# Performance work log

Hardware: AMD Instinct MI355X
Metric: run time of the kernel (lower is better)

The kernel has to match this reference:

```python
import jax, jax.numpy as jnp
import numpy as np

KEY_SIZE = 512


def setup_inputs() -> dict:
    key = jax.random.key(0)
    ks = jax.random.split(key, 4)
    B, T, C = 8, 2048, 512
    s = 0.02
    return {
        "x": jax.random.normal(ks[0], (B, T, C), dtype=jnp.float32),
        "Wq": jax.random.normal(ks[1], (KEY_SIZE, C), dtype=jnp.float32) * s,
        "bq": jnp.zeros((KEY_SIZE,), dtype=jnp.float32),
        "Wk": jax.random.normal(ks[2], (KEY_SIZE, C), dtype=jnp.float32) * s,
        "bk": jnp.zeros((KEY_SIZE,), dtype=jnp.float32),
        "Wv": jax.random.normal(ks[3], (KEY_SIZE, C), dtype=jnp.float32) * s,
        "bv": jnp.zeros((KEY_SIZE,), dtype=jnp.float32),
    }


def reference(x, Wq, bq, Wk, bk, Wv, bv):
    # x: [B, T, C]; Linear(y) = y @ W.T + b (torch convention)
    q = jnp.einsum("btc,kc->btk", x, Wq) + bq  # [B, T, K]
    k = jnp.einsum("btc,kc->btk", x, Wk) + bk  # [B, T, K]
    v = jnp.einsum("btc,vc->btv", x, Wv) + bv  # [B, T, V]

    scores = jnp.einsum("bqk,bsk->bqs", q, k)  # [B, Tq, Tk]
    T = x.shape[1]
    # mask[j, i] = 1 if i > j  -> strict upper triangle masked with -inf
    mask = jnp.triu(jnp.ones((T, T), dtype=bool), k=1)
    scores = jnp.where(mask[None, :, :], -jnp.inf, scores)
    # NOTE: original divides by sqrt(key_size) AFTER masking, and takes
    # softmax over dim=1 (the QUERY axis) — faithfully reproduced.
    probs = jax.nn.softmax(scores / jnp.sqrt(jnp.asarray(KEY_SIZE, scores.dtype)), axis=1)
    attn = jnp.einsum("bqs,bsv->bqv", probs, v)  # [B, T, V]
    return jnp.concatenate([x, attn], axis=2)  # [B, T, C + V]
```

## Files before the change

kernel.cpp:

```cpp
#include <hip/hip_runtime.h>

#define BATCH 8
#define TSEQ  2048
#define CDIM  512
#define MTOK  (BATCH*TSEQ)
#define NTRI  136

typedef __attribute__((ext_vector_type(8))) short bf16x8;
typedef __attribute__((ext_vector_type(4))) float f32x4;

__device__ __forceinline__ unsigned short f2bf(float f) {
    union { float f; unsigned int u; } v; v.f = f;
    unsigned int r = v.u + 0x7FFF + ((v.u >> 16) & 1);
    return (unsigned short)(r >> 16);
}
__device__ __forceinline__ float bfl(unsigned short u) {
    union { unsigned int i; float f; } v; v.i = ((unsigned int)u) << 16; return v.f;
}

__device__ __forceinline__ f32x4 fzero() { f32x4 z = {0.f, 0.f, 0.f, 0.f}; return z; }

__device__ __forceinline__ void gl2lds16(const void* g, void* l) {
    __builtin_amdgcn_global_load_lds(
        (const __attribute__((address_space(1))) unsigned int*)g,
        (__attribute__((address_space(3))) unsigned int*)l, 16, 0, 0);
}

__device__ __forceinline__ void stage_tile(const unsigned short* src, size_t ld,
                                           unsigned short* buf, int t) {
    const unsigned short* s0 = src + (size_t)(t >> 2) * ld + (t & 3) * 8;
    gl2lds16(s0, &buf[t * 8]);
    gl2lds16(s0 + (size_t)64 * ld, &buf[2048 + t * 8]);
}

__global__ __launch_bounds__(256) void k_convert_x(const float* __restrict__ x,
                                                   unsigned short* __restrict__ xb,
                                                   float* __restrict__ out) {
    int i = blockIdx.x * blockDim.x + threadIdx.x;
    float4 v = ((const float4*)x)[i];
    ushort4 o;
    o.x = f2bf(v.x); o.y = f2bf(v.y); o.z = f2bf(v.z); o.w = f2bf(v.w);
    ((ushort4*)xb)[i] = o;
    int e = i * 4;
    int row = e >> 9;
    int c   = e & 511;
    *(float4*)(out + (size_t)row * 1024 + c) = v;
}

__global__ __launch_bounds__(256) void k_convert_w3(const float* __restrict__ Wq,
                                                    const float* __restrict__ Wk,
                                                    const float* __restrict__ Wv,
                                                    unsigned short* __restrict__ wb) {
    int i = blockIdx.x * 256 + threadIdx.x;
    int m = i >> 16;
    const float* w = (m == 0) ? Wq : ((m == 1) ? Wk : Wv);
    float4 v = ((const float4*)w)[i & 65535];
    ushort4 o;
    o.x = f2bf(v.x); o.y = f2bf(v.y); o.z = f2bf(v.z); o.w = f2bf(v.w);
    ((ushort4*)wb)[i] = o;
}

__global__ __launch_bounds__(512, 2) void k_qkv(const unsigned short* __restrict__ xb,
                                                const unsigned short* __restrict__ Wcat,
                                                const float* __restrict__ bq,
                                                const float* __restrict__ bk,
                                                const float* __restrict__ bv,
                                                unsigned short* __restrict__ QKb,
                                                unsigned short* __restrict__ Vt) {
    __shared__ __align__(16) unsigned short lds[65536];
    int orig = blockIdx.x;
    int flat = (orig & 7) * 48 + (orig >> 3);
    int mt = flat / 6, nt = flat - mt * 6;
    int m0 = mt * 256, n0 = nt * 256;
    int t = threadIdx.x, w = t >> 6, lane = t & 63;
    int quad = lane >> 4, lane16 = lane & 15;
    int wr = w >> 2, wc = w & 3;
    int l3 = lane >> 3;
    int sl = (lane & 7) ^ l3;
    int rswz = (lane16 & 7) << 3;

    const unsigned short* Abase = xb + (size_t)m0 * 512;
    const unsigned short* Bbase = Wcat + (size_t)n0 * 512;

    f32x4 acc[8][4];
#pragma unroll
    for (int i = 0; i < 8; i++)
#pragma unroll
        for (int j = 0; j < 4; j++) acc[i][j] = fzero();

    auto stage = [&](const unsigned short* src, unsigned short* buf) {
#pragma unroll
        for (int i = 0; i < 4; ++i) {
            int q = i * 8 + w;
            gl2lds16(src + (size_t)(q * 8 + l3) * 512 + sl * 8,
                     &buf[q * 512 + lane * 8]);
        }
    };

    stage(Abase, &lds[0]);
    stage(Bbase, &lds[16384]);
    __syncthreads();

#pragma unroll
    for (int kt = 0; kt < 8; ++kt) {
        int c = kt & 1;
        if (kt + 1 < 8) {
            stage(Abase + (kt + 1) * 64, &lds[(c ^ 1) * 32768]);
            stage(Bbase + (kt + 1) * 64, &lds[(c ^ 1) * 32768 + 16384]);
        }
        const unsigned short* As = &lds[c * 32768];
        const unsigned short* Bs = As + 16384;

        bf16x8 bfr[4][2];
#pragma unroll
        for (int ni = 0; ni < 4; ++ni) {
            int row = wc * 64 + ni * 16 + lane16;
#pragma unroll
            for (int ks = 0; ks < 2; ++ks)
                bfr[ni][ks] = *(const bf16x8*)&Bs[row * 64 + ((ks * 32 + quad * 8) ^ rswz)];
        }
#pragma unroll
        for (int mh = 0; mh < 2; ++mh) {
            bf16x8 afr[4][2];
#pragma unroll
            for (int mi2 = 0; mi2 < 4; ++mi2) {
                int row = wr * 128 + mh * 64 + mi2 * 16 + lane16;
#pragma unroll
                for (int ks = 0; ks < 2; ++ks)
                    afr[mi2][ks] = *(const bf16x8*)&As[row * 64 + ((ks * 32 + quad * 8) ^ rswz)];
            }
            __builtin_amdgcn_s_setprio(1);
#pragma unroll
            for (int mi2 = 0; mi2 < 4; ++mi2)
#pragma unroll
                for (int ni = 0; ni < 4; ++ni)
#pragma unroll
                    for (int ks = 0; ks < 2; ++ks)
                        acc[mh * 4 + mi2][ni] = __builtin_amdgcn_mfma_f32_16x16x32_bf16(
                            afr[mi2][ks], bfr[ni][ks], acc[mh * 4 + mi2][ni], 0, 0, 0);
            __builtin_amdgcn_s_setprio(0);
        }
        __syncthreads();
    }

    int which = n0 >> 9;
    if (which < 2) {
        const float* bias = which ? bk : bq;
        unsigned short* T = &lds[w * 4608];
        int colBase = which * 512 + (n0 & 511) + wc * 64;
#pragma unroll
        for (int p = 0; p < 2; ++p) {
#pragma unroll
            for (int ni = 0; ni < 4; ++ni) {
                float bb = bias[(n0 & 511) + wc * 64 + ni * 16 + lane16];
#pragma unroll
                for (int mi2 = 0; mi2 < 4; ++mi2)
#pragma unroll
                    for (int r = 0; r < 4; ++r)
                        T[(mi2 * 16 + quad * 4 + r) * 72 + ni * 16 + lane16] =
                            f2bf(acc[p * 4 + mi2][ni][r] + bb);
            }
#pragma unroll
            for (int i = 0; i < 8; ++i) {
                int rl = i * 8 + l3;
                int cl = (lane & 7) * 8;
                int m = m0 + wr * 128 + p * 64 + rl;
                *(uint4*)(QKb + (size_t)m * 1024 + colBase + cl) = *(const uint4*)&T[rl * 72 + cl];
            }
        }
    } else {
        unsigned short* T = &lds[w * 4352];
        int b = m0 >> 11, tbase = (m0 & 2047) + wr * 128;
        int nv = (n0 & 511) + wc * 64;
#pragma unroll
        for (int p = 0; p < 2; ++p) {
#pragma unroll
            for (int j = 0; j < 2; ++j) {
                int ni = p * 2 + j;
                float bb = bv[nv + ni * 16 + lane16];
                int vl = j * 16 + lane16;
#pragma unroll
                for (int mi = 0; mi < 8; ++mi)
#pragma unroll
                    for (int r = 0; r < 4; ++r)
                        T[vl * 136 + mi * 16 + quad * 4 + r] = f2bf(acc[mi][ni][r] + bb);
            }
#pragma unroll
            for (int i = 0; i < 8; ++i) {
                int vl = i * 4 + quad;
                int tl = lane16 * 8;
                int v = nv + p * 32 + vl;
                *(uint4*)(Vt + ((size_t)(b * 512 + v)) * 2048 + tbase + tl) =
                    *(const uint4*)&T[vl * 136 + tl];
            }
        }
    }
}

__global__ __launch_bounds__(256) void k_score(const unsigned short* __restrict__ QKb,
                                               unsigned short* __restrict__ Pbuf,
                                               float* __restrict__ colsum) {
    __shared__ __align__(16) unsigned short lds[16384];
    int orig = blockIdx.x;
    int bb  = orig & 7;
    int idx = orig >> 3;
    int qt = (int)((sqrtf(8.0f * idx + 1.0f) - 1.0f) * 0.5f);
    while ((qt + 1) * (qt + 2) / 2 <= idx) qt++;
    while (qt * (qt + 1) / 2 > idx) qt--;
    int st = idx - qt * (qt + 1) / 2;
    int q0 = qt * 128, s0 = st * 128;

    int t = threadIdx.x, w = t >> 6, lane = t & 63, quad = lane >> 4, lane16 = lane & 15;
    int rowHalf = (w >> 1) * 64, colHalf = (w & 1) * 64;
    const unsigned short* Qrows = QKb + ((size_t)(bb * 2048 + q0)) * 1024;
    const unsigned short* Krows = QKb + ((size_t)(bb * 2048 + s0)) * 1024 + 512;

    f32x4 acc[4][4];
#pragma unroll
    for (int i = 0; i < 4; i++)
#pragma unroll
        for (int j = 0; j < 4; j++) acc[i][j] = fzero();

    stage_tile(Qrows, 1024, lds, t);
    stage_tile(Krows, 1024, lds + 4096, t);
    __syncthreads();
    int cur = 0;
    for (int k0 = 0; k0 < CDIM; k0 += 32) {
        unsigned short* As = lds + cur * 8192;
        unsigned short* Bs = As + 4096;
        if (k0 + 32 < CDIM) {
            unsigned short* An = lds + (cur ^ 1) * 8192;
            stage_tile(Qrows + k0 + 32, 1024, An, t);
            stage_tile(Krows + k0 + 32, 1024, An + 4096, t);
        }
        bf16x8 a[4], b[4];
#pragma unroll
        for (int mi = 0; mi < 4; mi++)
            a[mi] = *(const bf16x8*)&As[(rowHalf + mi * 16 + lane16) * 32 + quad * 8];
#pragma unroll
        for (int ni = 0; ni < 4; ni++)
            b[ni] = *(const bf16x8*)&Bs[(colHalf + ni * 16 + lane16) * 32 + quad * 8];
#pragma unroll
        for (int mi = 0; mi < 4; mi++)
#pragma unroll
            for (int ni = 0; ni < 4; ni++)
                acc[mi][ni] = __builtin_amdgcn_mfma_f32_16x16x32_bf16(a[mi], b[ni], acc[mi][ni], 0, 0, 0);
        __syncthreads();
        cur ^= 1;
    }

    const float scale = 0.044194173824159216f;
    unsigned short* T = &lds[w * 4096];
    float csum[4] = {0.f, 0.f, 0.f, 0.f};
#pragma unroll
    for (int ni = 0; ni < 4; ni++) {
        int s = s0 + colHalf + ni * 16 + lane16;
#pragma unroll
        for (int mi = 0; mi < 4; mi++)
#pragma unroll
            for (int r = 0; r < 4; r++) {
                int q = q0 + rowHalf + mi * 16 + quad * 4 + r;
                float p = 0.0f;
                if (s <= q) { p = __expf(acc[mi][ni][r] * scale); csum[ni] += p; }
                T[(mi * 16 + quad * 4 + r) * 64 + ni * 16 + lane16] = f2bf(p);
            }
    }
#pragma unroll
    for (int ni = 0; ni < 4; ni++) {
        float v = csum[ni];
        v += __shfl_xor(v, 16);
        v += __shfl_xor(v, 32);
        if (quad == 0)
            unsafeAtomicAdd(&colsum[bb * 2048 + s0 + colHalf + ni * 16 + lane16], v);
    }
    __syncthreads();
    unsigned short* tile = Pbuf + ((size_t)(bb * NTRI + idx)) * 16384;
#pragma unroll
    for (int i = 0; i < 8; i++) {
        int rl = i * 8 + (lane >> 3);
        int cl = (lane & 7) * 8;
        *(uint4*)(tile + (rowHalf + rl) * 128 + colHalf + cl) = *(const uint4*)&T[rl * 64 + cl];
    }
}

__global__ __launch_bounds__(256) void k_invcs(float* __restrict__ cs) {
    int i = blockIdx.x * 256 + threadIdx.x;
    cs[i] = 1.0f / cs[i];
}

__global__ __launch_bounds__(256) void k_vscale(unsigned short* __restrict__ Vt,
                                                const float* __restrict__ inv) {
    int idx = blockIdx.x * 256 + threadIdx.x;
    int s8  = idx & 255;
    int row = idx >> 8;
    int b   = row >> 9;
    uint4 raw = ((const uint4*)Vt)[idx];
    const float* ip = inv + b * TSEQ + s8 * 8;
    unsigned int rr[4] = {raw.x, raw.y, raw.z, raw.w};
    unsigned int oo[4];
#pragma unroll
    for (int j = 0; j < 4; j++) {
        float f0 = bfl((unsigned short)(rr[j] & 0xffff)) * ip[j * 2];
        float f1 = bfl((unsigned short)(rr[j] >> 16))    * ip[j * 2 + 1];
        oo[j] = (unsigned int)f2bf(f0) | ((unsigned int)f2bf(f1) << 16);
    }
    uint4 o = {oo[0], oo[1], oo[2], oo[3]};
    ((uint4*)Vt)[idx] = o;
}

__global__ __launch_bounds__(256) void k_attn(const unsigned short* __restrict__ Pbuf,
                                              const unsigned short* __restrict__ Vt,
                                              float* __restrict__ out) {
    __shared__ __align__(16) unsigned short lds[16384];
    int i = blockIdx.x;
    int slot = i & 255, half = i >> 8;
    int qt = half ? (15 - (slot >> 5)) : (slot >> 5);
    int bv = slot & 31;
    int bb = bv >> 2;
    int v0 = (bv & 3) * 128;
    int t = threadIdx.x, w = t >> 6, lane = t & 63, quad = lane >> 4, lane16 = lane & 15;
    int rowHalf = (w >> 1) * 64, colHalf = (w & 1) * 64;

    const unsigned short* Pb = Pbuf + ((size_t)(bb * NTRI + qt * (qt + 1) / 2)) * 16384;
    const unsigned short* Vb = Vt + ((size_t)(bb * 512 + v0)) * 2048;

    f32x4 acc[4][4];
#pragma unroll
    for (int ii = 0; ii < 4; ii++)
#pragma unroll
        for (int j = 0; j < 4; j++) acc[ii][j] = fzero();

    int Kend = (qt + 1) * 128;
    stage_tile(Pb, 128, lds, t);
    stage_tile(Vb, 2048, lds + 4096, t);
    __syncthreads();
    int cur = 0;
    for (int k0 = 0; k0 < Kend; k0 += 32) {
        unsigned short* As = lds + cur * 8192;
        unsigned short* Bs = As + 4096;
        int k1 = k0 + 32;
        if (k1 < Kend) {
            unsigned short* An = lds + (cur ^ 1) * 8192;
            stage_tile(Pb + (size_t)(k1 >> 7) * 16384 + (k1 & 127), 128, An, t);
            stage_tile(Vb + k1, 2048, An + 4096, t);
        }
        bf16x8 a[4], b[4];
#pragma unroll
        for (int mi = 0; mi < 4; mi++)
            a[mi] = *(const bf16x8*)&As[(rowHalf + mi * 16 + lane16) * 32 + quad * 8];
#pragma unroll
        for (int ni = 0; ni < 4; ni++)
            b[ni] = *(const bf16x8*)&Bs[(colHalf + ni * 16 + lane16) * 32 + quad * 8];
#pragma unroll
        for (int mi = 0; mi < 4; mi++)
#pragma unroll
            for (int ni = 0; ni < 4; ni++)
                acc[mi][ni] = __builtin_amdgcn_mfma_f32_16x16x32_bf16(a[mi], b[ni], acc[mi][ni], 0, 0, 0);
        __syncthreads();
        cur ^= 1;
    }

#pragma unroll
    for (int mi = 0; mi < 4; mi++)
#pragma unroll
        for (int ni = 0; ni < 4; ni++)
#pragma unroll
            for (int r = 0; r < 4; r++) {
                int q = qt * 128 + rowHalf + mi * 16 + quad * 4 + r;
                int v = v0 + colHalf + ni * 16 + lane16;
                out[((size_t)(bb * 2048 + q)) * 1024 + 512 + v] = acc[mi][ni][r];
            }
}

extern "C" void kernel_launch(void* const* d_in, const int* in_sizes, int n_in,
                              void* d_out, int out_size, void* d_ws, size_t ws_size,
                              hipStream_t stream) {
    const float* x  = (const float*)d_in[0];
    const float* Wq = (const float*)d_in[1];
    const float* bq = (const float*)d_in[2];
    const float* Wk = (const float*)d_in[3];
    const float* bk = (const float*)d_in[4];
    const float* Wv = (const float*)d_in[5];
    const float* bv = (const float*)d_in[6];
    float* out = (float*)d_out;

    char* ws = (char*)d_ws;
    size_t off = 0;
    auto alloc = [&](size_t bytes) -> void* {
        void* p = ws + off;
        off += (bytes + 255) & ~(size_t)255;
        return p;
    };
    unsigned short* QKb = (unsigned short*)alloc((size_t)MTOK * 1024 * 2);
    unsigned short* Vt  = (unsigned short*)alloc((size_t)MTOK * CDIM * 2);
    float* colsum = (float*)alloc((size_t)BATCH * TSEQ * 4);
    size_t mark = off;
    unsigned short* Wcat = (unsigned short*)alloc((size_t)3 * CDIM * CDIM * 2);
    unsigned short* xb   = (unsigned short*)alloc((size_t)MTOK * CDIM * 2);
    unsigned short* Pbuf = (unsigned short*)(ws + mark);
    (void)ws_size;

    k_convert_x<<<(MTOK * CDIM / 4) / 256, 256, 0, stream>>>(x, xb, out);
    k_convert_w3<<<(3 * CDIM * CDIM / 4) / 256, 256, 0, stream>>>(Wq, Wk, Wv, Wcat);

    k_qkv<<<384, 512, 0, stream>>>(xb, Wcat, bq, bk, bv, QKb, Vt);

    hipMemsetAsync(colsum, 0, (size_t)BATCH * TSEQ * 4, stream);
    k_score<<<1088, 256, 0, stream>>>(QKb, Pbuf, colsum);

    k_invcs<<<(BATCH * TSEQ) / 256, 256, 0, stream>>>(colsum);
    k_vscale<<<(MTOK * CDIM / 8) / 256, 256, 0, stream>>>(Vt, colsum);

    k_attn<<<512, 256, 0, stream>>>(Pbuf, Vt, out);
}
```

Measured before the change: 217.3 us.

## Restructure QKV projection GEMM main loop into fine-grained half-tile pipelined schedule

Rewrites the QKV projection GEMM K-loop as an 8-wave ping-pong style schedule. Loads are staged in half-tiles interleaved between four quadrant MFMA blocks, with explicit vmcnt/lgkmcnt waits and sched barriers. The goal is to overlap global-to-LDS loads and LDS fragment reads with MFMA work instead of staging whole tiles and syncing once per K step. It also adds a syncthreads in the V-transpose epilogue. The cost is many more barriers per iteration and a hand-tuned wait count scheme that could stall or race if miscounted.

```diff
diff --git a/kernel.cpp b/kernel.cpp
--- a/kernel.cpp
+++ b/kernel.cpp
@@ -32,6 +32,14 @@
     gl2lds16(s0, &buf[t * 8]);
     gl2lds16(s0 + (size_t)64 * ld, &buf[2048 + t * 8]);
 }
+
+#define LGKM0() do { asm volatile("s_waitcnt lgkmcnt(0)" ::: "memory"); \
+                     __builtin_amdgcn_sched_barrier(0); } while (0)
+#define VMCNT(n) do { asm volatile("s_waitcnt vmcnt(" #n ")" ::: "memory"); \
+                      __builtin_amdgcn_sched_barrier(0); } while (0)
+#define BARRIER() do { __builtin_amdgcn_sched_barrier(0); \
+                       __builtin_amdgcn_s_barrier(); \
+                       __builtin_amdgcn_sched_barrier(0); } while (0)
 
 __global__ __launch_bounds__(256) void k_convert_x(const float* __restrict__ x,
                                                    unsigned short* __restrict__ xb,
@@ -88,60 +96,109 @@
 #pragma unroll
         for (int j = 0; j < 4; j++) acc[i][j] = fzero();
 
-    auto stage = [&](const unsigned short* src, unsigned short* buf) {
-#pragma unroll
-        for (int i = 0; i < 4; ++i) {
+    auto stage_half = [&](const unsigned short* panel, int r0, int kt,
+                          unsigned short* buf) {
+#pragma unroll
+        for (int i = 0; i < 2; ++i) {
             int q = i * 8 + w;
-            gl2lds16(src + (size_t)(q * 8 + l3) * 512 + sl * 8,
+            gl2lds16(panel + (size_t)(r0 + q * 8 + l3) * 512 + kt * 64 + sl * 8,
                      &buf[q * 512 + lane * 8]);
         }
     };
-
-    stage(Abase, &lds[0]);
-    stage(Bbase, &lds[16384]);
+    auto ldsA = [&](int c, int h) { return &lds[c * 32768 + h * 8192]; };
+    auto ldsB = [&](int c, int h) { return &lds[c * 32768 + 16384 + h * 8192]; };
+
+    stage_half(Bbase, 0,   0, ldsB(0, 0));
+    stage_half(Bbase, 128, 0, ldsB(0, 1));
+    stage_half(Abase, 0,   0, ldsA(0, 0));
+    stage_half(Abase, 128, 0, ldsA(0, 1));
+    __builtin_amdgcn_sched_barrier(0);
+    stage_half(Bbase, 0,   1, ldsB(1, 0));
+    stage_half(Bbase, 128, 1, ldsB(1, 1));
+    stage_half(Abase, 0,   1, ldsA(1, 0));
+    VMCNT(6);
+    BARRIER();
+
+    bf16x8 afr[4][2];
+    bf16x8 bfr[2][2][2];
+
+    auto ldA = [&](int c, int mh) {
+        const unsigned short* As = &lds[c * 32768];
+        int rowb = wr * 128 + mh * 64 + lane16;
+#pragma unroll
+        for (int mi = 0; mi < 4; ++mi)
+#pragma unroll
+            for (int ks = 0; ks < 2; ++ks)
+                afr[mi][ks] = *(const bf16x8*)&As[(rowb + mi * 16) * 64 +
+                                                  ((ks * 32 + quad * 8) ^ rswz)];
+    };
+    auto ldB = [&](int c) {
+        const unsigned short* Bs = &lds[c * 32768 + 16384];
+        int rowb = wc * 64 + lane16;
+#pragma unroll
+        for (int ni = 0; ni < 4; ++ni)
+#pragma unroll
+            for (int ks = 0; ks < 2; ++ks)
+                bfr[ni >> 1][ni & 1][ks] = *(const bf16x8*)&Bs[(rowb + ni * 16) * 64 +
+                                                  ((ks * 32 + quad * 8) ^ rswz)];
+    };
+    auto quadmma = [&](int mh, int nh) {
+        __builtin_amdgcn_s_setprio(1);
+#pragma unroll
+        for (int mi = 0; mi < 4; ++mi)
+#pragma unroll
+            for (int nin = 0; nin < 2; ++nin)
+#pragma unroll
+                for (int ks = 0; ks < 2; ++ks)
+                    acc[mh * 4 + mi][nh * 2 + nin] = __builtin_amdgcn_mfma_f32_16x16x32_bf16(
+                        afr[mi][ks], bfr[nh][nin][ks], acc[mh * 4 + mi][nh * 2 + nin], 0, 0, 0);
+        __builtin_amdgcn_s_setprio(0);
+    };
+
+#pragma unroll
+    for (int i = 0; i < 4; ++i) {
+        const int tE = 2 * i + 2;
+        const int tO = 2 * i + 3;
+        ldA(0, 0); ldB(0);
+        stage_half(Abase, 128, 2 * i + 1, ldsA(1, 1));
+        BARRIER(); LGKM0();
+        quadmma(0, 0);
+        BARRIER();
+        if (tE < 8) stage_half(Bbase, 0, tE, ldsB(0, 0));
+        BARRIER();
+        quadmma(0, 1);
+        BARRIER();
+        ldA(0, 1);
+        if (tE < 8) stage_half(Bbase, 128, tE, ldsB(0, 1));
+        BARRIER(); LGKM0();
+        quadmma(1, 0);
+        BARRIER();
+        if (tE < 8) stage_half(Abase, 0, tE, ldsA(0, 0));
+        if (i < 3) { VMCNT(6); } else { VMCNT(0); }
+        BARRIER();
+        quadmma(1, 1);
+        BARRIER();
+        ldA(1, 0); ldB(1);
+        if (tE < 8) stage_half(Abase, 128, tE, ldsA(0, 1));
+        BARRIER(); LGKM0();
+        quadmma(0, 0);
+        BARRIER();
+        if (tO < 8) stage_half(Bbase, 0, tO, ldsB(1, 0));
+        BARRIER();
+        quadmma(0, 1);
+        BARRIER();
+        ldA(1, 1);
+        if (tO < 8) stage_half(Bbase, 128, tO, ldsB(1, 1));
+        BARRIER(); LGKM0();
+        quadmma(1, 0);
+        BARRIER();
+        if (tO < 8) stage_half(Abase, 0, tO, ldsA(1, 0));
+        if (i < 3) { VMCNT(6); }
+        BARRIER();
+        quadmma(1, 1);
+        BARRIER();
+    }
     __syncthreads();
-
-#pragma unroll
-    for (int kt = 0; kt < 8; ++kt) {
-        int c = kt & 1;
-        if (kt + 1 < 8) {
-            stage(Abase + (kt + 1) * 64, &lds[(c ^ 1) * 32768]);
-            stage(Bbase + (kt + 1) * 64, &lds[(c ^ 1) * 32768 + 16384]);
-        }
-        const unsigned short* As = &lds[c * 32768];
-        const unsigned short* Bs = As + 16384;
-
-        bf16x8 bfr[4][2];
-#pragma unroll
-        for (int ni = 0; ni < 4; ++ni) {
-            int row = wc * 64 + ni * 16 + lane16;
-#pragma unroll
-            for (int ks = 0; ks < 2; ++ks)
-                bfr[ni][ks] = *(const bf16x8*)&Bs[row * 64 + ((ks * 32 + quad * 8) ^ rswz)];
-        }
-#pragma unroll
-        for (int mh = 0; mh < 2; ++mh) {
-            bf16x8 afr[4][2];
-#pragma unroll
-            for (int mi2 = 0; mi2 < 4; ++mi2) {
-                int row = wr * 128 + mh * 64 + mi2 * 16 + lane16;
-#pragma unroll
-                for (int ks = 0; ks < 2; ++ks)
-                    afr[mi2][ks] = *(const bf16x8*)&As[row * 64 + ((ks * 32 + quad * 8) ^ rswz)];
-            }
-            __builtin_amdgcn_s_setprio(1);
-#pragma unroll
-            for (int mi2 = 0; mi2 < 4; ++mi2)
-#pragma unroll
-                for (int ni = 0; ni < 4; ++ni)
-#pragma unroll
-                    for (int ks = 0; ks < 2; ++ks)
-                        acc[mh * 4 + mi2][ni] = __builtin_amdgcn_mfma_f32_16x16x32_bf16(
-                            afr[mi2][ks], bfr[ni][ks], acc[mh * 4 + mi2][ni], 0, 0, 0);
-            __builtin_amdgcn_s_setprio(0);
-        }
-        __syncthreads();
-    }
 
     int which = n0 >> 9;
     if (which < 2) {
@@ -193,6 +250,7 @@
                 *(uint4*)(Vt + ((size_t)(b * 512 + v)) * 2048 + tbase + tl) =
                     *(const uint4*)&T[vl * 136 + tl];
             }
+            __syncthreads();
         }
     }
 }
```

New measurement: 216.3 us. Within noise of the previous version (-0.5%).
